# Performance work log

Measured on AMD Instinct MI355X. Metric: run time of the kernel, lower is better.

## Reference

```python
import jax, jax.numpy as jnp
import numpy as np

NUM_HEADS = 16  # config.num_attention_heads


def setup_inputs() -> dict:
    key = jax.random.key(0)
    k0, k1, k2 = jax.random.split(key, 3)
    B, S, D = 2, 2048, 2048
    hd = D // NUM_HEADS  # 128
    hidden_states = jax.random.normal(k0, (B, S, D), dtype=jnp.float32)
    c_attn_w = jax.random.normal(k1, (D + 2 * hd, D), dtype=jnp.float32) * 0.02
    c_attn_b = jnp.zeros((D + 2 * hd,), dtype=jnp.float32)
    c_proj_w = jax.random.normal(k2, (D, D), dtype=jnp.float32) * 0.02
    c_proj_b = jnp.zeros((D,), dtype=jnp.float32)
    return {
        "hidden_states": hidden_states,
        "c_attn_w": c_attn_w,
        "c_attn_b": c_attn_b,
        "c_proj_w": c_proj_w,
        "c_proj_b": c_proj_b,
    }


def reference(hidden_states, c_attn_w, c_attn_b, c_proj_w, c_proj_b):
    B, S, D = hidden_states.shape
    H = NUM_HEADS
    hd = D // H
    scale = hd ** -0.5

    # fused QKV projection: [B,S,D] -> [B,S,D+2*hd]
    qkv = hidden_states @ c_attn_w.T + c_attn_b
    # multi-query split: per-head Q, single shared K and V
    q = qkv[..., :D].reshape(B, S, H, hd)        # [B,S,H,hd]
    k = qkv[..., D:D + hd]                       # [B,S,hd]
    v = qkv[..., D + hd:]                        # [B,S,hd]

    # attention scores (full matrix materialized, like the baddbmm path)
    scores = jnp.einsum('bqhd,bkd->bhqk', q, k) * scale  # [B,H,S,S]
    causal = jnp.tril(jnp.ones((S, S), dtype=bool))
    scores = jnp.where(causal, scores, jnp.finfo(scores.dtype).min)
    attn = jax.nn.softmax(scores, axis=-1)

    # context: shared V broadcast across heads
    ctx = jnp.einsum('bhqk,bkd->bqhd', attn, v).reshape(B, S, D)
    out = ctx @ c_proj_w.T + c_proj_b
    return out
```

## Files before the change

kernel.cpp:

```cpp
#include <hip/hip_runtime.h>
#include <hip/hip_bf16.h>
#include <math.h>

typedef unsigned short u16;
typedef __attribute__((ext_vector_type(8))) __bf16 bf16x8;
typedef __attribute__((ext_vector_type(4))) float f32x4;

__device__ inline u16 f2bf(float f) {
  union { float f; unsigned u; } x; x.f = f;
  unsigned r = x.u + 0x7fffu + ((x.u >> 16) & 1u);
  return (u16)(r >> 16);
}

__device__ inline unsigned cvtpk(float lo, float hi) {
  unsigned r;
  asm("v_cvt_pk_bf16_f32 %0, %1, %2" : "=v"(r) : "v"(lo), "v"(hi));
  return r;
}

__device__ inline float fexp2(float x) {
  float r;
  asm("v_exp_f32 %0, %1" : "=v"(r) : "v"(x));
  return r;
}

__device__ inline void async16(const void* g, void* l) {
  __builtin_amdgcn_global_load_lds(
      (const __attribute__((address_space(1))) void*)g,
      (__attribute__((address_space(3))) void*)l, 16, 0, 0);
}

__global__ __launch_bounds__(256) void cast_bf16_kernel(
    const float* __restrict__ in, u16* __restrict__ out, int n4) {
  int i = blockIdx.x * 256 + threadIdx.x;
  if (i >= n4) return;
  float4 v = ((const float4*)in)[i];
  u16 o0 = f2bf(v.x), o1 = f2bf(v.y), o2 = f2bf(v.z), o3 = f2bf(v.w);
  unsigned lo = (unsigned)o0 | ((unsigned)o1 << 16);
  unsigned hi = (unsigned)o2 | ((unsigned)o3 << 16);
  ((uint2*)out)[i] = make_uint2(lo, hi);
}

__global__ __launch_bounds__(256) void vt_kernel(
    const u16* __restrict__ qkv, u16* __restrict__ vt) {
  __shared__ u16 tile[32][136];
  const int t = threadIdx.x;
  const int b = blockIdx.x >> 6;
  const int S0 = (blockIdx.x & 63) * 32;
  const int s_l = t >> 3, dg = t & 7;
  const u16* src = qkv + ((size_t)b * 2048 + S0 + s_l) * 2304 + 2176 + dg * 16;
  *(uint4*)&tile[s_l][dg * 16] = *(const uint4*)src;
  *(uint4*)&tile[s_l][dg * 16 + 8] = *(const uint4*)(src + 8);
  __syncthreads();
  const int d = t >> 1, sh = t & 1;
  u16 buf[16];
#pragma unroll
  for (int j = 0; j < 16; ++j) buf[j] = tile[sh * 16 + j][d];
  u16* dst = vt + ((size_t)b * 128 + d) * 2048 + S0 + sh * 16;
  *(uint4*)dst = *(uint4*)&buf[0];
  *(uint4*)(dst + 8) = *(uint4*)&buf[8];
}

template <bool BF16OUT>
__global__ __launch_bounds__(256) void gemm_bt(
    const u16* __restrict__ A, const u16* __restrict__ Bw,
    const float* __restrict__ bias, void* __restrict__ Cout,
    int M, int N, int K, int qcols, float qscale) {
  __shared__ u16 As[128 * 64];
  __shared__ u16 Bs[128 * 64];
  const int t = threadIdx.x;
  const int w = t >> 6;
  const int lane = t & 63;
  const int lq = lane >> 4, lr = lane & 15;
  const long brow = (long)blockIdx.y * 128;
  const long bcol = (long)blockIdx.x * 128;
  const int wr = (w >> 1) * 64, wc = (w & 1) * 64;
  f32x4 acc[4][4] = {};

  int rA[4], cA[4];
#pragma unroll
  for (int it = 0; it < 4; ++it) {
    int ci = it * 256 + t;
    rA[it] = ci >> 3;
    cA[it] = (ci & 7) ^ (rA[it] & 7);
  }

  for (int kt = 0; kt < K; kt += 64) {
#pragma unroll
    for (int it = 0; it < 4; ++it) {
      const u16* srcA = A + (brow + rA[it]) * (long)K + kt + cA[it] * 8;
      async16(srcA, (char*)As + (it * 256 + w * 64) * 16);
      const u16* srcB = Bw + (bcol + rA[it]) * (long)K + kt + cA[it] * 8;
      async16(srcB, (char*)Bs + (it * 256 + w * 64) * 16);
    }
    __syncthreads();
#pragma unroll
    for (int kb = 0; kb < 2; ++kb) {
      bf16x8 af[4], bfr[4];
#pragma unroll
      for (int m = 0; m < 4; ++m) {
        int row = wr + m * 16 + lr;
        int byte = (row * 128 + kb * 64 + lq * 16) ^ ((row & 7) << 4);
        af[m] = *(const bf16x8*)((const char*)As + byte);
      }
#pragma unroll
      for (int n = 0; n < 4; ++n) {
        int row = wc + n * 16 + lr;
        int byte = (row * 128 + kb * 64 + lq * 16) ^ ((row & 7) << 4);
        bfr[n] = *(const bf16x8*)((const char*)Bs + byte);
      }
#pragma unroll
      for (int m = 0; m < 4; ++m)
#pragma unroll
        for (int n = 0; n < 4; ++n)
          acc[m][n] = __builtin_amdgcn_mfma_f32_16x16x32_bf16(
              af[m], bfr[n], acc[m][n], 0, 0, 0);
    }
    __syncthreads();
  }

#pragma unroll
  for (int m = 0; m < 4; ++m) {
    long row0 = brow + wr + m * 16 + lq * 4;
#pragma unroll
    for (int n = 0; n < 4; ++n) {
      long col = bcol + wc + n * 16 + lr;
      float bv = bias[col];
      float cs = (col < qcols) ? qscale : 1.f;
#pragma unroll
      for (int j = 0; j < 4; ++j) {
        float v = (acc[m][n][j] + bv) * cs;
        if (BF16OUT)
          ((u16*)Cout)[(row0 + j) * N + col] = f2bf(v);
        else
          ((float*)Cout)[(row0 + j) * N + col] = v;
      }
    }
  }
}

__global__ __launch_bounds__(256, 2) void attn_kernel(
    const u16* __restrict__ qkv, const u16* __restrict__ vt,
    u16* __restrict__ ctx) {
  __shared__ u16 Kl[2][64 * 136];
  __shared__ u16 Vl[2][128 * 72];
  __shared__ u16 Pl[4][16 * 72];

  const int t = threadIdx.x;
  const int w = t >> 6;
  const int lane = t & 63;
  const int lq = lane >> 4, lr = lane & 15;
  const int lkey = lq * 4;
  const int bid = blockIdx.x;
  const int qtid = bid >> 5;
  const int qt = (qtid < 8) ? (15 - qtid) : (qtid - 8);
  const int hb = bid & 31;
  const int h = hb & 15;
  const int b = hb >> 4;
  const int s0w = qt * 128 + w * 32;
  const size_t qb = (size_t)b * 2048 * 2304;

  bf16x8 qg[2][4];
#pragma unroll
  for (int s = 0; s < 2; ++s)
#pragma unroll
    for (int kc = 0; kc < 4; ++kc)
      qg[s][kc] = *(const bf16x8*)(qkv + qb +
                                   (size_t)(s0w + s * 16 + lr) * 2304 +
                                   h * 128 + kc * 32 + lq * 8);

  const u16* kp[5];
  const u16* vp[5];
#pragma unroll
  for (int ii = 0; ii < 5; ++ii) {
    int I = 4 * ii + w;
    {
      int pp = I * 1024 + lane * 16;
      int row = pp / 272;
      int rem = pp - row * 272;
      int ch = (rem < 256) ? (rem >> 4) : 0;
      if (row > 63) row = 63;
      kp[ii] = qkv + qb + (size_t)row * 2304 + 2048 + ch * 8;
    }
    {
      int pp = I * 1024 + lane * 16;
      int row = pp / 144;
      int rem = pp - row * 144;
      int ch = (rem < 128) ? (rem >> 4) : 0;
      if (row > 127) row = 127;
      vp[ii] = vt + ((size_t)b * 128 + row) * 2048 + ch * 8;
    }
  }
  char* const KlB = (char*)&Kl[0][0];
  char* const VlB = (char*)&Vl[0][0];

  auto stage = [&](int buf) {
    char* kd = KlB + buf * 17408;
    char* vd = VlB + buf * 18432;
#pragma unroll
    for (int ii = 0; ii < 5; ++ii) {
      int I = 4 * ii + w;
      if (I < 17) {
        async16(kp[ii], kd + I * 1024);
        kp[ii] += 64 * 2304;
      }
    }
#pragma unroll
    for (int ii = 0; ii < 5; ++ii) {
      int I = 4 * ii + w;
      if (I < 18) {
        async16(vp[ii], vd + I * 1024);
        vp[ii] += 64;
      }
    }
  };

  const int loK = lr * 272 + lq * 16;
  const int loV = lr * 144 + lq * 16;
  char* const pb = (char*)&Pl[w][0];
  char* const pw0 = pb + lr * 144 + lq * 8;
  const char* const PL = pb + lr * 144 + lq * 16;

  float mreg[2] = {-INFINITY, -INFINITY};
  float lreg[2] = {0.f, 0.f};
  f32x4 o[2][8] = {};
  const int ntiles = 2 * qt + 2;

  stage(0);
  __syncthreads();

  int cur = 0;
  for (int j2 = 0; j2 < ntiles; ++j2) {
    const int kvb = j2 * 64;
    if (j2 + 1 < ntiles) stage(cur ^ 1);
    if (kvb <= s0w + 31) {
      const char* KL = KlB + cur * 17408 + loK;
      const char* VL = VlB + cur * 18432 + loV;
      const bool maskT = (kvb + 63 > s0w);

      f32x4 sc[2][4] = {};
#pragma unroll
      for (int g = 0; g < 4; ++g)
#pragma unroll
        for (int kc = 0; kc < 4; ++kc) {
          bf16x8 kf = *(const bf16x8*)(KL + g * 4352 + kc * 64);
          sc[0][g] = __builtin_amdgcn_mfma_f32_16x16x32_bf16(kf, qg[0][kc],
                                                             sc[0][g], 0, 0, 0);
          sc[1][g] = __builtin_amdgcn_mfma_f32_16x16x32_bf16(kf, qg[1][kc],
                                                             sc[1][g], 0, 0, 0);
        }

      bf16x8 pa[2][2];
#pragma unroll
      for (int s = 0; s < 2; ++s) {
        float vv[16];
#pragma unroll
        for (int u = 0; u < 16; ++u) vv[u] = sc[s][u >> 2][u & 3];
        if (maskT) {
          const int qrel = s0w + s * 16 + lr - kvb;
#pragma unroll
          for (int g = 0; g < 4; ++g)
#pragma unroll
            for (int r = 0; r < 4; ++r)
              if (g * 16 + lkey + r > qrel) vv[g * 4 + r] = -INFINITY;
        }
        float mx = vv[0];
#pragma unroll
        for (int u = 1; u < 16; ++u) mx = fmaxf(mx, vv[u]);
        mx = fmaxf(mx, __shfl_xor(mx, 16));
        mx = fmaxf(mx, __shfl_xor(mx, 32));
        float mn = mreg[s];
        if (__any(mx > mn + 8.f)) {
          float mu = fmaxf(mn, mx);
          float alpha = fexp2(mn - mu);
          mreg[s] = mu;
          mn = mu;
          lreg[s] *= alpha;
          float a0 = __shfl(alpha, lkey + 0);
          float a1 = __shfl(alpha, lkey + 1);
          float a2 = __shfl(alpha, lkey + 2);
          float a3 = __shfl(alpha, lkey + 3);
#pragma unroll
          for (int n = 0; n < 8; ++n) {
            o[s][n][0] *= a0;
            o[s][n][1] *= a1;
            o[s][n][2] *= a2;
            o[s][n][3] *= a3;
          }
        }
        float rs = 0.f;
#pragma unroll
        for (int g = 0; g < 4; ++g)
#pragma unroll
          for (int rp = 0; rp < 2; ++rp) {
            float p0 = fexp2(vv[g * 4 + 2 * rp] - mn);
            float p1 = fexp2(vv[g * 4 + 2 * rp + 1] - mn);
            rs += p0 + p1;
            *(unsigned*)(pw0 + g * 32 + rp * 4) = cvtpk(p0, p1);
          }
        rs += __shfl_xor(rs, 16);
        rs += __shfl_xor(rs, 32);
        lreg[s] += rs;
        pa[s][0] = *(const bf16x8*)(PL);
        pa[s][1] = *(const bf16x8*)(PL + 64);
      }

#pragma unroll
      for (int n = 0; n < 8; ++n) {
        bf16x8 vf0 = *(const bf16x8*)(VL + n * 2304);
        bf16x8 vf1 = *(const bf16x8*)(VL + n * 2304 + 64);
        o[0][n] = __builtin_amdgcn_mfma_f32_16x16x32_bf16(pa[0][0], vf0,
                                                          o[0][n], 0, 0, 0);
        o[0][n] = __builtin_amdgcn_mfma_f32_16x16x32_bf16(pa[0][1], vf1,
                                                          o[0][n], 0, 0, 0);
        o[1][n] = __builtin_amdgcn_mfma_f32_16x16x32_bf16(pa[1][0], vf0,
                                                          o[1][n], 0, 0, 0);
        o[1][n] = __builtin_amdgcn_mfma_f32_16x16x32_bf16(pa[1][1], vf1,
                                                          o[1][n], 0, 0, 0);
      }
    }
    __syncthreads();
    cur ^= 1;
  }

#pragma unroll
  for (int s = 0; s < 2; ++s) {
    float inv = 1.f / lreg[s];
    float iv[4];
    iv[0] = __shfl(inv, lkey + 0);
    iv[1] = __shfl(inv, lkey + 1);
    iv[2] = __shfl(inv, lkey + 2);
    iv[3] = __shfl(inv, lkey + 3);
#pragma unroll
    for (int r = 0; r < 4; ++r) {
      size_t rowoff =
          ((size_t)b * 2048 + s0w + s * 16 + lkey + r) * 2048 + h * 128;
#pragma unroll
      for (int n = 0; n < 8; ++n)
        ctx[rowoff + n * 16 + lr] = f2bf(o[s][n][r] * iv[r]);
    }
  }
}

extern "C" void kernel_launch(void* const* d_in, const int* in_sizes, int n_in,
                              void* d_out, int out_size, void* d_ws,
                              size_t ws_size, hipStream_t stream) {
  (void)in_sizes; (void)n_in; (void)out_size; (void)ws_size;
  const float* hs = (const float*)d_in[0];
  const float* attn_w = (const float*)d_in[1];
  const float* attn_b = (const float*)d_in[2];
  const float* proj_w = (const float*)d_in[3];
  const float* proj_b = (const float*)d_in[4];
  float* out = (float*)d_out;

  u16* hs_b = (u16*)d_ws;
  u16* aw_b = hs_b + (size_t)4096 * 2048;
  u16* pw_b = aw_b + (size_t)2304 * 2048;
  u16* qkv_b = pw_b + (size_t)2048 * 2048;
  u16* vt_b = qkv_b + (size_t)4096 * 2304;
  u16* ctx_b = vt_b + (size_t)2 * 128 * 2048;

  const float qscale = 0.08838834764831845f * 1.4426950408889634f;

  cast_bf16_kernel<<<8192, 256, 0, stream>>>(hs, hs_b, 2097152);
  cast_bf16_kernel<<<4608, 256, 0, stream>>>(attn_w, aw_b, 1179648);
  cast_bf16_kernel<<<4096, 256, 0, stream>>>(proj_w, pw_b, 1048576);

  gemm_bt<true><<<dim3(18, 32), 256, 0, stream>>>(hs_b, aw_b, attn_b, qkv_b,
                                                  4096, 2304, 2048, 2048,
                                                  qscale);
  vt_kernel<<<128, 256, 0, stream>>>(qkv_b, vt_b);
  attn_kernel<<<512, 256, 0, stream>>>(qkv_b, vt_b, ctx_b);
  gemm_bt<false><<<dim3(16, 32), 256, 0, stream>>>(ctx_b, pw_b, proj_b, out,
                                                   4096, 2048, 2048, 0, 1.f);
}
```

Measured before the change: 210.2 us.

## Double-buffer GEMM LDS tiles and remap blocks for XCD locality

```diff
diff --git a/kernel.cpp b/kernel.cpp
--- a/kernel.cpp
+++ b/kernel.cpp
@@ -66,14 +66,25 @@
     const u16* __restrict__ A, const u16* __restrict__ Bw,
     const float* __restrict__ bias, void* __restrict__ Cout,
     int M, int N, int K, int qcols, float qscale) {
-  __shared__ u16 As[128 * 64];
-  __shared__ u16 Bs[128 * 64];
+  __shared__ u16 As[2][128 * 64];
+  __shared__ u16 Bs[2][128 * 64];
   const int t = threadIdx.x;
   const int w = t >> 6;
   const int lane = t & 63;
   const int lq = lane >> 4, lr = lane & 15;
-  const long brow = (long)blockIdx.y * 128;
-  const long bcol = (long)blockIdx.x * 128;
+
+  int bx = blockIdx.x, by = blockIdx.y;
+  const int gx = gridDim.x, gy = gridDim.y;
+  if ((gx & 1) == 0 && (gy & 3) == 0) {
+    const int cw = gx >> 1, ch = gy >> 2;
+    int id = by * gx + bx;
+    int xcd = id & 7, j = id >> 3;
+    bx = (xcd & 1) * cw + j % cw;
+    by = (xcd >> 1) * ch + j / cw;
+  }
+
+  const long brow = (long)by * 128;
+  const long bcol = (long)bx * 128;
   const int wr = (w >> 1) * 64, wc = (w & 1) * 64;
   f32x4 acc[4][4] = {};
 
@@ -85,15 +96,29 @@
     cA[it] = (ci & 7) ^ (rA[it] & 7);
   }
 
-  for (int kt = 0; kt < K; kt += 64) {
+  char* const AsB = (char*)&As[0][0];
+  char* const BsB = (char*)&Bs[0][0];
+
+  auto stage = [&](int buf, int kt) {
+    char* ad = AsB + buf * 16384;
+    char* bd = BsB + buf * 16384;
 #pragma unroll
     for (int it = 0; it < 4; ++it) {
       const u16* srcA = A + (brow + rA[it]) * (long)K + kt + cA[it] * 8;
-      async16(srcA, (char*)As + (it * 256 + w * 64) * 16);
+      async16(srcA, ad + (it * 256 + w * 64) * 16);
       const u16* srcB = Bw + (bcol + rA[it]) * (long)K + kt + cA[it] * 8;
-      async16(srcB, (char*)Bs + (it * 256 + w * 64) * 16);
-    }
-    __syncthreads();
+      async16(srcB, bd + (it * 256 + w * 64) * 16);
+    }
+  };
+
+  stage(0, 0);
+  __syncthreads();
+
+  int cur = 0;
+  for (int kt = 0; kt < K; kt += 64) {
+    if (kt + 64 < K) stage(cur ^ 1, kt + 64);
+    const char* Ab = AsB + cur * 16384;
+    const char* Bb = BsB + cur * 16384;
 #pragma unroll
     for (int kb = 0; kb < 2; ++kb) {
       bf16x8 af[4], bfr[4];
@@ -101,13 +126,13 @@
       for (int m = 0; m < 4; ++m) {
         int row = wr + m * 16 + lr;
         int byte = (row * 128 + kb * 64 + lq * 16) ^ ((row & 7) << 4);
-        af[m] = *(const bf16x8*)((const char*)As + byte);
+        af[m] = *(const bf16x8*)(Ab + byte);
       }
 #pragma unroll
       for (int n = 0; n < 4; ++n) {
         int row = wc + n * 16 + lr;
         int byte = (row * 128 + kb * 64 + lq * 16) ^ ((row & 7) << 4);
-        bfr[n] = *(const bf16x8*)((const char*)Bs + byte);
+        bfr[n] = *(const bf16x8*)(Bb + byte);
       }
 #pragma unroll
       for (int m = 0; m < 4; ++m)
@@ -117,6 +142,7 @@
               af[m], bfr[n], acc[m][n], 0, 0, 0);
     }
     __syncthreads();
+    cur ^= 1;
   }
 
 #pragma unroll
```

Result: faster. 195.4 us (-7.0%).
